# Kernel tuning notes

Hardware: AMD Instinct MI355X
Metric: run time of the kernel (lower is better)

The kernel has to match this reference:

```python
import jax, jax.numpy as jnp
import numpy as np

# Configuration mirroring init_kwargs
B, H, W = 64, 40, 40          # batch, grid (image 1280 / stride 32)
A, C = 5, 80                  # anchors per cell, classes
MAX_BOXES = 100               # max_detection_boxes
SCORE_THR = 0.001             # nms_score_threshold
IOU_THR = 0.5                 # nms_iou_threshold


def setup_inputs() -> dict:
    key = jax.random.key(0)
    k1, k2 = jax.random.split(key)
    predictions = jax.random.normal(k1, (B, H, W, A * (5 + C)), dtype=jnp.float32)
    # anchor (w, h) in grid-cell units, positive
    anchors = jax.random.uniform(k2, (A, 2), dtype=jnp.float32, minval=0.5, maxval=8.0)
    return {"predictions": predictions, "anchors": anchors}


def decode_yolo(predictions, anchors):
    """YOLOv2-style decode -> normalized corner boxes and per-class scores."""
    b, h, w, _ = predictions.shape
    p = predictions.reshape(b, h, w, A, 5 + C)
    gy, gx = jnp.meshgrid(jnp.arange(h, dtype=jnp.float32),
                          jnp.arange(w, dtype=jnp.float32), indexing="ij")
    grid = jnp.stack([gx, gy], axis=-1)[None, :, :, None, :]   # [1,h,w,1,2]
    dims = jnp.array([w, h], dtype=jnp.float32)
    xy = (jax.nn.sigmoid(p[..., 0:2]) + grid) / dims           # normalized centers
    wh = jnp.exp(p[..., 2:4]) * anchors / dims                 # normalized sizes
    conf = jax.nn.sigmoid(p[..., 4:5])
    probs = jax.nn.softmax(p[..., 5:], axis=-1)
    scores = conf * probs                                      # [b,h,w,A,C]
    boxes = jnp.concatenate([xy - wh * 0.5, xy + wh * 0.5], axis=-1)  # x1,y1,x2,y2
    return boxes.reshape(b, -1, 4), scores.reshape(b, -1, C)


def nms_single(boxes, scores_all):
    """Greedy per-class NMS for one image. boxes [N,4], scores_all [N,C]."""
    cls_scores = jnp.max(scores_all, axis=-1)
    classes = jnp.argmax(scores_all, axis=-1)
    s0 = jnp.where(cls_scores > SCORE_THR, cls_scores, -1.0)
    area = jnp.maximum(boxes[:, 2] - boxes[:, 0], 0.0) * \
           jnp.maximum(boxes[:, 3] - boxes[:, 1], 0.0)

    def step(s, _):
        idx = jnp.argmax(s)
        sc = s[idx]
        box = boxes[idx]
        x1 = jnp.maximum(box[0], boxes[:, 0]); y1 = jnp.maximum(box[1], boxes[:, 1])
        x2 = jnp.minimum(box[2], boxes[:, 2]); y2 = jnp.minimum(box[3], boxes[:, 3])
        inter = jnp.maximum(x2 - x1, 0.0) * jnp.maximum(y2 - y1, 0.0)
        box_area = jnp.maximum(box[2] - box[0], 0.0) * jnp.maximum(box[3] - box[1], 0.0)
        iou = inter / (area + box_area - inter + 1e-8)
        suppress = (iou > IOU_THR) & (classes == classes[idx])
        s_new = jnp.where(suppress, -1.0, s).at[idx].set(-1.0)
        valid = sc > 0.0
        out_box = jnp.where(valid, box, 0.0)
        out_sc = jnp.where(valid, sc, 0.0)
        out_cl = jnp.where(valid, classes[idx], -1)
        return s_new, (out_box, out_sc, out_cl)

    _, (ob, osc, ocl) = jax.lax.scan(step, s0, None, length=MAX_BOXES)
    return ob, osc, ocl  # [MAX_BOXES,4], [MAX_BOXES], [MAX_BOXES]


def reference(predictions, anchors):
    boxes, scores = decode_yolo(predictions, anchors)
    sel_boxes, sel_scores, sel_classes = jax.vmap(nms_single)(boxes, scores)
    return sel_boxes, sel_scores, sel_classes
```

## Files before the change

### kernel.cpp

```cpp
#include <hip/hip_runtime.h>
#include <math.h>

#define B 64
#define H 40
#define W 40
#define A 5
#define C 80
#define NBOX (H*W*A)
#define FEAT (5+C)
#define MAXB 100
#define SCORE_THR 0.001f
#define IOU_THR 0.5f

#define DEC_BOXES 64
#define DEC_THREADS 64
#define DEC_LDS4 1408

#define HBINS 10240
#define BINBASE 119808
#define TARGET 512

#define BK 48
#define RCAP 1024

typedef unsigned long long u64;
typedef unsigned int u32;

__global__ __launch_bounds__(DEC_THREADS) void decode_kernel(
    const float* __restrict__ pred, const float* __restrict__ anchors,
    float* __restrict__ boxes_ws, float* __restrict__ s_ws, int* __restrict__ cls_ws,
    int* __restrict__ ghist)
{
    __shared__ float lds[DEC_LDS4 * 4];
    const int tid = threadIdx.x;
    const int base_box = blockIdx.x * DEC_BOXES;

    {
        const float4* src4 = (const float4*)pred;
        const long long base4 = (long long)base_box * FEAT / 4;
        const long long TOT4  = (long long)B * NBOX * FEAT / 4;
        #pragma unroll
        for (int i = 0; i < 22; ++i) {
            long long g4 = base4 + i*64 + tid;
            if (g4 >= TOT4) g4 = TOT4 - 1;
            __builtin_amdgcn_global_load_lds(
                (const __attribute__((address_space(1))) void*)(src4 + g4),
                (__attribute__((address_space(3))) void*)((char*)lds + i*1024),
                16, 0, 0);
        }
    }
    __syncthreads();

    const int box = base_box + tid;
    const float* l = lds + tid * FEAT;

    int img  = box / NBOX;
    int n    = box - img * NBOX;
    int cell = n / A;
    int a    = n - cell * A;
    int gx   = cell % W;
    int gy   = cell / W;

    float tx = l[0], ty = l[1], tw = l[2], th = l[3], tc = l[4];

    float lg[C];
    #pragma unroll
    for (int i = 0; i < C; ++i) lg[i] = l[5+i];

    float sx = 1.f / (1.f + expf(-tx));
    float sy = 1.f / (1.f + expf(-ty));
    float cx = (sx + (float)gx) / (float)W;
    float cy = (sy + (float)gy) / (float)H;
    float aw = anchors[a*2+0], ah = anchors[a*2+1];
    float bw = expf(tw) * aw / (float)W;
    float bh = expf(th) * ah / (float)H;
    float conf = 1.f / (1.f + expf(-tc));

    float mm[8];
    #pragma unroll
    for (int w = 0; w < 8; ++w) mm[w] = lg[w];
    #pragma unroll
    for (int i = 8; i < C; ++i) mm[i & 7] = fmaxf(mm[i & 7], lg[i]);
    float m = fmaxf(fmaxf(fmaxf(mm[0],mm[1]),fmaxf(mm[2],mm[3])),
                    fmaxf(fmaxf(mm[4],mm[5]),fmaxf(mm[6],mm[7])));

    float sum = 0.f;
    float bv[4] = {-1.f,-1.f,-1.f,-1.f};
    int   bi[4] = {0,0,0,0};
    #pragma unroll
    for (int i = 0; i < C; ++i) {
        float e = expf(lg[i] - m);
        sum += e;
        int w = i & 3;
        if (e > bv[w]) { bv[w] = e; bi[w] = i; }
    }
    float best_e = bv[0]; int best_c = bi[0];
    #pragma unroll
    for (int w = 1; w < 4; ++w) {
        if (bv[w] > best_e || (bv[w] == best_e && bi[w] < best_c)) { best_e = bv[w]; best_c = bi[w]; }
    }

    float score = conf * (best_e / sum);
    float s0 = (score > SCORE_THR) ? score : -1.0f;

    float x1 = cx - bw*0.5f, y1 = cy - bh*0.5f;
    float x2 = cx + bw*0.5f, y2 = cy + bh*0.5f;

    ((float4*)boxes_ws)[box] = make_float4(x1, y1, x2, y2);
    s_ws[box] = s0;
    cls_ws[box] = best_c;

    if (s0 > 0.f) {
        int b = (int)(__float_as_uint(s0) >> 13) - BINBASE;
        b = max(0, min(HBINS-1, b));
        atomicAdd(&ghist[img*HBINS + b], 1);
    }
}

__global__ __launch_bounds__(1024) void scanscatter_kernel(
    const int* __restrict__ ghist,
    const float* __restrict__ boxes_ws, const float* __restrict__ s_ws,
    const int* __restrict__ cls_ws,
    int* __restrict__ bucketCnt, u64* __restrict__ bucketKey,
    float4* __restrict__ bucketBox)
{
    __shared__ int wavesum[16];
    __shared__ int tbin_s;
    const int img  = blockIdx.x;
    const int tid  = threadIdx.x;
    const int lane = tid & 63;
    const int wid  = tid >> 6;
    const int* gh = ghist + img * HBINS;

    if (tid < C)  bucketCnt[img*C + tid] = 0;
    if (tid == 0) tbin_s = 0;
    __syncthreads();

    int sum_r = 0;
    {
        int base = HBINS - 10*(tid+1);
        #pragma unroll
        for (int q = 0; q < 10; ++q) sum_r += gh[base + q];
    }
    int incl = sum_r;
    #pragma unroll
    for (int off = 1; off < 64; off <<= 1) {
        int o = __shfl_up(incl, off);
        if (lane >= off) incl += o;
    }
    if (lane == 63) wavesum[wid] = incl;
    __syncthreads();
    {
        int wbase = 0;
        for (int w = 0; w < wid; ++w) wbase += wavesum[w];
        int excl = wbase + incl - sum_r;
        if (excl < TARGET && excl + sum_r >= TARGET) {
            int cum = excl;
            for (int q = 0; q < 10; ++q) {
                int b = HBINS - 10*tid - 1 - q;
                cum += gh[b];
                if (cum >= TARGET) { tbin_s = b; break; }
            }
        }
    }
    __syncthreads();
    const int tb = tbin_s;

    const long long ib = (long long)img * NBOX;
    #pragma unroll
    for (int k = 0; k < 8; ++k) {
        int n = tid + k*1024;
        if (n < NBOX) {
            float s = s_ws[ib + n];
            if (s > 0.f) {
                int b = (int)(__float_as_uint(s) >> 13) - BINBASE;
                b = max(0, min(HBINS-1, b));
                if (b >= tb) {
                    int c  = cls_ws[ib + n];
                    int bb = img*C + c;
                    int pos = atomicAdd(&bucketCnt[bb], 1);
                    if (pos < BK) {
                        u64 key = ((u64)__float_as_uint(s) << 32)
                                | ((u64)(NBOX - n) << 19)
                                | ((u64)pos << 13) | (u64)c;
                        bucketKey[bb*BK + pos] = key;
                        bucketBox[bb*BK + pos] = ((const float4*)boxes_ws)[ib + n];
                    }
                }
            }
        }
    }
}

__device__ __forceinline__ u64 wave_max_u64(u64 v) {
    #define STAGE(CTRL, RMASK) { \
        u32 lo = (u32)v, hi = (u32)(v >> 32); \
        u32 tlo = (u32)__builtin_amdgcn_update_dpp(0, (int)lo, CTRL, RMASK, 0xf, true); \
        u32 thi = (u32)__builtin_amdgcn_update_dpp(0, (int)hi, CTRL, RMASK, 0xf, true); \
        u64 t = ((u64)thi << 32) | (u64)tlo; \
        if (t > v) v = t; \
    }
    STAGE(0x111, 0xf)
    STAGE(0x112, 0xf)
    STAGE(0x114, 0xf)
    STAGE(0x118, 0xf)
    STAGE(0x142, 0xa)
    STAGE(0x143, 0xc)
    #undef STAGE
    u32 flo = (u32)__builtin_amdgcn_readlane((int)(u32)v, 63);
    u32 fhi = (u32)__builtin_amdgcn_readlane((int)(v >> 32), 63);
    return ((u64)fhi << 32) | (u64)flo;
}

__global__ __launch_bounds__(1024) void nmsrank_kernel(
    const int* __restrict__ bucketCnt, const u64* __restrict__ bucketKey,
    const float4* __restrict__ bucketBox, float* __restrict__ out)
{
    __shared__ u64 skeys[C*BK];
    __shared__ u64 ckeys[RCAP];
    __shared__ int cnt;
    const int img  = blockIdx.x;
    const int tid  = threadIdx.x;
    const int lane = tid & 63;
    const int wid  = tid >> 6;

    if (tid == 0) cnt = 0;

    for (int q = 0; q < 5; ++q) {
        const int c  = wid*5 + q;
        const int bb = img*C + c;
        const int n  = min(bucketCnt[bb], BK);

        u64 key = 0, keep = 0;
        float x1=0.f, y1=0.f, x2=0.f, y2=0.f, ar=0.f;
        if (lane < n) {
            key = bucketKey[bb*BK + lane];
            float4 b4 = bucketBox[bb*BK + lane];
            x1=b4.x; y1=b4.y; x2=b4.z; y2=b4.w;
            ar = fmaxf(x2-x1,0.f)*fmaxf(y2-y1,0.f);
        }

        for (int t = 0; t < BK; ++t) {
            u64 bk = wave_max_u64(key);
            if (bk == 0) break;
            int sl = (int)((bk >> 13) & 63);
            float sx1 = __shfl(x1, sl), sy1 = __shfl(y1, sl);
            float sx2 = __shfl(x2, sl), sy2 = __shfl(y2, sl);
            float sarea = fmaxf(sx2-sx1,0.f)*fmaxf(sy2-sy1,0.f);

            if (lane == sl) {
                keep = key;
                key = 0;
            } else if (key != 0) {
                float ix1 = fmaxf(sx1, x1);
                float iy1 = fmaxf(sy1, y1);
                float ix2 = fminf(sx2, x2);
                float iy2 = fminf(sy2, y2);
                float inter = fmaxf(ix2-ix1,0.f)*fmaxf(iy2-iy1,0.f);
                float iou = inter / (ar + sarea - inter + 1e-8f);
                if (iou > IOU_THR) key = 0;
            }
        }

        if (lane < BK) skeys[c*BK + lane] = keep;
    }
    __syncthreads();

    for (int i = tid; i < C*BK; i += 1024) {
        u64 k = skeys[i];
        if (k != 0) {
            int p = atomicAdd(&cnt, 1);
            if (p < RCAP) ckeys[p] = k;
        }
    }
    __syncthreads();
    const int m = min(cnt, RCAP);

    float* out_boxes  = out;
    float* out_scores = out + B*MAXB*4;
    float* out_cls    = out + B*MAXB*5;

    for (int i = tid; i < m; i += 1024) {
        u64 mine = ckeys[i];
        int r = 0;
        for (int j = 0; j < m; ++j) r += (ckeys[j] > mine) ? 1 : 0;
        if (r < MAXB) {
            int c   = (int)(mine & 127);
            int pos = (int)((mine >> 13) & 63);
            float4 b4 = bucketBox[((long long)img*C + c)*BK + pos];
            int o = img*MAXB + r;
            out_boxes[o*4+0] = b4.x; out_boxes[o*4+1] = b4.y;
            out_boxes[o*4+2] = b4.z; out_boxes[o*4+3] = b4.w;
            out_scores[o] = __uint_as_float((u32)(mine >> 32));
            out_cls[o]    = (float)c;
        }
    }

    int base = min(m, MAXB);
    for (int r = base + tid; r < MAXB; r += 1024) {
        int o = img*MAXB + r;
        out_boxes[o*4+0]=0.f; out_boxes[o*4+1]=0.f;
        out_boxes[o*4+2]=0.f; out_boxes[o*4+3]=0.f;
        out_scores[o]=0.f;
        out_cls[o]=-1.f;
    }
}

extern "C" void kernel_launch(void* const* d_in, const int* in_sizes, int n_in,
                              void* d_out, int out_size, void* d_ws, size_t ws_size,
                              hipStream_t stream) {
    const float* pred    = (const float*)d_in[0];
    const float* anchors = (const float*)d_in[1];
    float* out = (float*)d_out;

    char* p = (char*)d_ws;
    float*  boxes_ws  = (float*)p;              p += (size_t)B*NBOX*4*sizeof(float);
    float*  s_ws      = (float*)p;              p += (size_t)B*NBOX*sizeof(float);
    int*    cls_ws    = (int*)p;                p += (size_t)B*NBOX*sizeof(int);
    int*    bucketCnt = (int*)p;                p += (size_t)B*C*sizeof(int);
    u64*    bucketKey = (u64*)p;                p += (size_t)B*C*BK*sizeof(u64);
    float4* bucketBox = (float4*)p;             p += (size_t)B*C*BK*sizeof(float4);
    int*    ghist     = (int*)p;

    hipMemsetAsync(ghist, 0, (size_t)B*HBINS*sizeof(int), stream);
    decode_kernel<<<(B*NBOX)/DEC_BOXES, DEC_THREADS, 0, stream>>>(
        pred, anchors, boxes_ws, s_ws, cls_ws, ghist);
    scanscatter_kernel<<<B, 1024, 0, stream>>>(
        ghist, boxes_ws, s_ws, cls_ws, bucketCnt, bucketKey, bucketBox);
    nmsrank_kernel<<<B, 1024, 0, stream>>>(
        bucketCnt, bucketKey, bucketBox, out);
}
```

Before: 297.5 us.

## Fuse histogram, threshold scan, bucketing and NMS into one per-image kernel

```diff
diff --git a/kernel.cpp b/kernel.cpp
--- a/kernel.cpp
+++ b/kernel.cpp
@@ -28,8 +28,7 @@
 
 __global__ __launch_bounds__(DEC_THREADS) void decode_kernel(
     const float* __restrict__ pred, const float* __restrict__ anchors,
-    float* __restrict__ boxes_ws, float* __restrict__ s_ws, int* __restrict__ cls_ws,
-    int* __restrict__ ghist)
+    float* __restrict__ boxes_ws, float* __restrict__ s_ws, int* __restrict__ cls_ws)
 {
     __shared__ float lds[DEC_LDS4 * 4];
     const int tid = threadIdx.x;
@@ -109,87 +108,6 @@
     ((float4*)boxes_ws)[box] = make_float4(x1, y1, x2, y2);
     s_ws[box] = s0;
     cls_ws[box] = best_c;
-
-    if (s0 > 0.f) {
-        int b = (int)(__float_as_uint(s0) >> 13) - BINBASE;
-        b = max(0, min(HBINS-1, b));
-        atomicAdd(&ghist[img*HBINS + b], 1);
-    }
-}
-
-__global__ __launch_bounds__(1024) void scanscatter_kernel(
-    const int* __restrict__ ghist,
-    const float* __restrict__ boxes_ws, const float* __restrict__ s_ws,
-    const int* __restrict__ cls_ws,
-    int* __restrict__ bucketCnt, u64* __restrict__ bucketKey,
-    float4* __restrict__ bucketBox)
-{
-    __shared__ int wavesum[16];
-    __shared__ int tbin_s;
-    const int img  = blockIdx.x;
-    const int tid  = threadIdx.x;
-    const int lane = tid & 63;
-    const int wid  = tid >> 6;
-    const int* gh = ghist + img * HBINS;
-
-    if (tid < C)  bucketCnt[img*C + tid] = 0;
-    if (tid == 0) tbin_s = 0;
-    __syncthreads();
-
-    int sum_r = 0;
-    {
-        int base = HBINS - 10*(tid+1);
-        #pragma unroll
-        for (int q = 0; q < 10; ++q) sum_r += gh[base + q];
-    }
-    int incl = sum_r;
-    #pragma unroll
-    for (int off = 1; off < 64; off <<= 1) {
-        int o = __shfl_up(incl, off);
-        if (lane >= off) incl += o;
-    }
-    if (lane == 63) wavesum[wid] = incl;
-    __syncthreads();
-    {
-        int wbase = 0;
-        for (int w = 0; w < wid; ++w) wbase += wavesum[w];
-        int excl = wbase + incl - sum_r;
-        if (excl < TARGET && excl + sum_r >= TARGET) {
-            int cum = excl;
-            for (int q = 0; q < 10; ++q) {
-                int b = HBINS - 10*tid - 1 - q;
-                cum += gh[b];
-                if (cum >= TARGET) { tbin_s = b; break; }
-            }
-        }
-    }
-    __syncthreads();
-    const int tb = tbin_s;
-
-    const long long ib = (long long)img * NBOX;
-    #pragma unroll
-    for (int k = 0; k < 8; ++k) {
-        int n = tid + k*1024;
-        if (n < NBOX) {
-            float s = s_ws[ib + n];
-            if (s > 0.f) {
-                int b = (int)(__float_as_uint(s) >> 13) - BINBASE;
-                b = max(0, min(HBINS-1, b));
-                if (b >= tb) {
-                    int c  = cls_ws[ib + n];
-                    int bb = img*C + c;
-                    int pos = atomicAdd(&bucketCnt[bb], 1);
-                    if (pos < BK) {
-                        u64 key = ((u64)__float_as_uint(s) << 32)
-                                | ((u64)(NBOX - n) << 19)
-                                | ((u64)pos << 13) | (u64)c;
-                        bucketKey[bb*BK + pos] = key;
-                        bucketBox[bb*BK + pos] = ((const float4*)boxes_ws)[ib + n];
-                    }
-                }
-            }
-        }
-    }
 }
 
 __device__ __forceinline__ u64 wave_max_u64(u64 v) {
@@ -212,30 +130,108 @@
     return ((u64)fhi << 32) | (u64)flo;
 }
 
-__global__ __launch_bounds__(1024) void nmsrank_kernel(
-    const int* __restrict__ bucketCnt, const u64* __restrict__ bucketKey,
-    const float4* __restrict__ bucketBox, float* __restrict__ out)
+__global__ __launch_bounds__(1024) void selnmsrank_kernel(
+    const float* __restrict__ boxes_ws, const float* __restrict__ s_ws,
+    const int* __restrict__ cls_ws, float* __restrict__ out)
 {
-    __shared__ u64 skeys[C*BK];
-    __shared__ u64 ckeys[RCAP];
+    __shared__ __align__(16) char smem[HBINS * 4];
+    int* hist  = (int*)smem;
+    u64* bkey  = (u64*)smem;
+    u64* ckeys = (u64*)(smem + 30720);
+    int* bcnt  = (int*)(smem + 38912);
+    __shared__ int wavesum[16];
+    __shared__ int tbin_s;
     __shared__ int cnt;
+
     const int img  = blockIdx.x;
     const int tid  = threadIdx.x;
     const int lane = tid & 63;
     const int wid  = tid >> 6;
-
-    if (tid == 0) cnt = 0;
+    const long long ib = (long long)img * NBOX;
+
+    #pragma unroll
+    for (int q = 0; q < HBINS/1024; ++q) hist[tid + q*1024] = 0;
+    if (tid == 0) { tbin_s = 0; cnt = 0; }
+    __syncthreads();
+
+    float sc_r[8];
+    #pragma unroll
+    for (int k = 0; k < 8; ++k) {
+        int j = tid + k*1024;
+        float s = (j < NBOX) ? s_ws[ib + j] : -1.f;
+        sc_r[k] = s;
+        if (s > 0.f) {
+            int b = (int)(__float_as_uint(s) >> 13) - BINBASE;
+            b = max(0, min(HBINS-1, b));
+            atomicAdd(&hist[b], 1);
+        }
+    }
+    __syncthreads();
+
+    int sum_r = 0;
+    {
+        int base = HBINS - 10*(tid+1);
+        #pragma unroll
+        for (int q = 0; q < 10; ++q) sum_r += hist[base + q];
+    }
+    int incl = sum_r;
+    #pragma unroll
+    for (int off = 1; off < 64; off <<= 1) {
+        int o = __shfl_up(incl, off);
+        if (lane >= off) incl += o;
+    }
+    if (lane == 63) wavesum[wid] = incl;
+    __syncthreads();
+    {
+        int wbase = 0;
+        for (int w = 0; w < wid; ++w) wbase += wavesum[w];
+        int excl = wbase + incl - sum_r;
+        if (excl < TARGET && excl + sum_r >= TARGET) {
+            int cum = excl;
+            for (int q = 0; q < 10; ++q) {
+                int b = HBINS - 10*tid - 1 - q;
+                cum += hist[b];
+                if (cum >= TARGET) { tbin_s = b; break; }
+            }
+        }
+    }
+    __syncthreads();
+    const int tb = tbin_s;
+
+    if (tid < C) bcnt[tid] = 0;
+    __syncthreads();
+
+    #pragma unroll
+    for (int k = 0; k < 8; ++k) {
+        int j = tid + k*1024;
+        float s = sc_r[k];
+        if (j < NBOX && s > 0.f) {
+            int b = (int)(__float_as_uint(s) >> 13) - BINBASE;
+            b = max(0, min(HBINS-1, b));
+            if (b >= tb) {
+                int c = cls_ws[ib + j];
+                int pos = atomicAdd(&bcnt[c], 1);
+                if (pos < BK) {
+                    u64 key = ((u64)__float_as_uint(s) << 32)
+                            | ((u64)(NBOX - j) << 19)
+                            | ((u64)pos << 13) | (u64)c;
+                    bkey[c*BK + pos] = key;
+                }
+            }
+        }
+    }
+    __syncthreads();
 
     for (int q = 0; q < 5; ++q) {
         const int c  = wid*5 + q;
-        const int bb = img*C + c;
-        const int n  = min(bucketCnt[bb], BK);
+        const int nb = min(bcnt[c], BK);
 
         u64 key = 0, keep = 0;
         float x1=0.f, y1=0.f, x2=0.f, y2=0.f, ar=0.f;
-        if (lane < n) {
-            key = bucketKey[bb*BK + lane];
-            float4 b4 = bucketBox[bb*BK + lane];
+        if (lane < nb) {
+            key = bkey[c*BK + lane];
+            int bidx = NBOX - (int)((key >> 19) & 0x1FFF);
+            float4 b4 = ((const float4*)boxes_ws)[ib + bidx];
             x1=b4.x; y1=b4.y; x2=b4.z; y2=b4.w;
             ar = fmaxf(x2-x1,0.f)*fmaxf(y2-y1,0.f);
         }
@@ -262,12 +258,12 @@
             }
         }
 
-        if (lane < BK) skeys[c*BK + lane] = keep;
+        if (lane < BK) bkey[c*BK + lane] = keep;
     }
     __syncthreads();
 
     for (int i = tid; i < C*BK; i += 1024) {
-        u64 k = skeys[i];
+        u64 k = bkey[i];
         if (k != 0) {
             int p = atomicAdd(&cnt, 1);
             if (p < RCAP) ckeys[p] = k;
@@ -285,9 +281,9 @@
         int r = 0;
         for (int j = 0; j < m; ++j) r += (ckeys[j] > mine) ? 1 : 0;
         if (r < MAXB) {
-            int c   = (int)(mine & 127);
-            int pos = (int)((mine >> 13) & 63);
-            float4 b4 = bucketBox[((long long)img*C + c)*BK + pos];
+            int c    = (int)(mine & 127);
+            int bidx = NBOX - (int)((mine >> 19) & 0x1FFF);
+            float4 b4 = ((const float4*)boxes_ws)[ib + bidx];
             int o = img*MAXB + r;
             out_boxes[o*4+0] = b4.x; out_boxes[o*4+1] = b4.y;
             out_boxes[o*4+2] = b4.z; out_boxes[o*4+3] = b4.w;
@@ -316,17 +312,10 @@
     char* p = (char*)d_ws;
     float*  boxes_ws  = (float*)p;              p += (size_t)B*NBOX*4*sizeof(float);
     float*  s_ws      = (float*)p;              p += (size_t)B*NBOX*sizeof(float);
-    int*    cls_ws    = (int*)p;                p += (size_t)B*NBOX*sizeof(int);
-    int*    bucketCnt = (int*)p;                p += (size_t)B*C*sizeof(int);
-    u64*    bucketKey = (u64*)p;                p += (size_t)B*C*BK*sizeof(u64);
-    float4* bucketBox = (float4*)p;             p += (size_t)B*C*BK*sizeof(float4);
-    int*    ghist     = (int*)p;
-
-    hipMemsetAsync(ghist, 0, (size_t)B*HBINS*sizeof(int), stream);
+    int*    cls_ws    = (int*)p;
+
     decode_kernel<<<(B*NBOX)/DEC_BOXES, DEC_THREADS, 0, stream>>>(
-        pred, anchors, boxes_ws, s_ws, cls_ws, ghist);
-    scanscatter_kernel<<<B, 1024, 0, stream>>>(
-        ghist, boxes_ws, s_ws, cls_ws, bucketCnt, bucketKey, bucketBox);
-    nmsrank_kernel<<<B, 1024, 0, stream>>>(
-        bucketCnt, bucketKey, bucketBox, out);
+        pred, anchors, boxes_ws, s_ws, cls_ws);
+    selnmsrank_kernel<<<B, 1024, 0, stream>>>(
+        boxes_ws, s_ws, cls_ws, out);
 }
```

Result: faster. 283.6 us (-4.7%).
